# Performance work log

Hardware: AMD Instinct MI355X
Metric: run time of the kernel (lower is better)

The kernel has to match this reference:

```python
import jax, jax.numpy as jnp
import numpy as np

N_QUBITS = 3
MAX_LAYERS = 15
Q_DEPTH = 2


def _apply_ry(state, theta, axis):
    """Apply RY(theta) to qubit `axis` (axes 1..3 of state [B,2,2,2]).
    theta: scalar (shared weight) or [B] (per-sample angle). RY is real.
    """
    st = jnp.moveaxis(state, axis, 1)
    s0, s1 = st[:, 0], st[:, 1]  # [B,2,2]
    c = jnp.cos(theta / 2)
    s = jnp.sin(theta / 2)
    c = c.reshape(c.shape + (1,) * (s0.ndim - c.ndim))
    s = s.reshape(s.shape + (1,) * (s0.ndim - s.ndim))
    new = jnp.stack([c * s0 - s * s1, s * s0 + c * s1], axis=1)
    return jnp.moveaxis(new, 1, axis)


def _cnot(state, ctrl_ax, tgt_ax):
    """CNOT with control/target given as state axes (1..3): flip target where control=1."""
    st = jnp.moveaxis(state, (ctrl_ax, tgt_ax), (1, 2))
    new = jnp.stack([st[:, 0], st[:, 1, ::-1]], axis=1)
    return jnp.moveaxis(new, (1, 2), (ctrl_ax, tgt_ax))


def _quantum_circuit(q_in, q_params):
    """Batched simulation of the PennyLane q_net: H layer, RY(q_in),
    then q_depth x [entangle(CNOT(0,1),CNOT(1,2)); RY(q_weights[k+1])].
    Returns <Z_j> for j=0..2, shape [B, 3]. All gates are real-valued."""
    B = q_in.shape[0]
    qw = q_params.reshape(MAX_LAYERS, N_QUBITS)
    # Hadamards on |000> -> uniform real superposition
    state = jnp.full((B, 2, 2, 2), 1.0 / np.sqrt(8.0), dtype=q_in.dtype)
    for j in range(N_QUBITS):
        state = _apply_ry(state, q_in[:, j], j + 1)
    for k in range(Q_DEPTH):
        state = _cnot(state, 1, 2)  # CNOT(wires=[0,1])
        state = _cnot(state, 2, 3)  # CNOT(wires=[1,2])
        for j in range(N_QUBITS):
            state = _apply_ry(state, qw[k + 1, j], j + 1)
    p = state * state  # probabilities (real amplitudes)
    signs = jnp.array([1.0, -1.0], dtype=p.dtype)
    z = [jnp.sum(jnp.moveaxis(p, j + 1, 1) * signs[None, :, None, None], axis=(1, 2, 3))
         for j in range(N_QUBITS)]
    return jnp.stack(z, axis=-1)  # [B, 3]


def setup_inputs() -> dict:
    key = jax.random.key(0)
    ks = jax.random.split(key, 6)
    B, F, NQ, NOUT = 65536, 512, N_QUBITS, 100
    return {
        "input_features": jax.random.normal(ks[0], (B, F), dtype=jnp.float32),
        "pre_W": jax.random.normal(ks[1], (NQ, F), dtype=jnp.float32) * 0.04,
        "pre_b": jax.random.normal(ks[2], (NQ,), dtype=jnp.float32) * 0.04,
        "q_params": 0.01 * jax.random.normal(ks[3], (MAX_LAYERS * NQ,), dtype=jnp.float32),
        "post_W": jax.random.normal(ks[4], (NOUT, NQ), dtype=jnp.float32) * 0.5,
        "post_b": jax.random.normal(ks[5], (NOUT,), dtype=jnp.float32) * 0.5,
    }


def reference(input_features, pre_W, pre_b, q_params, post_W, post_b):
    pre_out = input_features @ pre_W.T + pre_b          # [B, 3]
    q_in = jnp.tanh(pre_out) * (np.pi / 2.0)             # [B, 3]
    q_out = _quantum_circuit(q_in, q_params)             # [B, 3]
    return q_out @ post_W.T + post_b                     # [B, 100]
```

## Files before the change

### kernel.cpp

```cpp
#include <hip/hip_runtime.h>
#include <math.h>

#define FDIM 512
#define TILE 8
#define WPB  4
#define SPB  (TILE * WPB)

#define RYPAIR(x, y, c, s) { float n0_ = (c)*(x) - (s)*(y); float n1_ = (s)*(x) + (c)*(y); (x) = n0_; (y) = n1_; }
#define SWAPF(x, y) { float t_ = (x); (x) = (y); (y) = t_; }

#define MERGE(x, y, mask) {                       \
    const bool hi_ = (lane & (mask));             \
    float keep_ = hi_ ? (y) : (x);                \
    float send_ = hi_ ? (x) : (y);                \
    (x) = keep_ + __shfl_xor(send_, (mask)); }

__global__ __launch_bounds__(256) void qnet_v3(
    const float4* __restrict__ in4,
    const float4* __restrict__ preW4,
    const float*  __restrict__ preb,
    const float*  __restrict__ qp,
    const float*  __restrict__ postW,
    const float*  __restrict__ postb,
    float2*       __restrict__ out,
    int B)
{
    const int tid  = threadIdx.x;
    const int lane = tid & 63;
    const int wave = tid >> 6;

    const float4 w0a = preW4[lane],       w0b = preW4[64 + lane];
    const float4 w1a = preW4[128 + lane], w1b = preW4[192 + lane];
    const float4 w2a = preW4[256 + lane], w2b = preW4[320 + lane];

    const float pb0 = preb[0], pb1 = preb[1], pb2 = preb[2];

    float cw[2][3], sw[2][3];
    #pragma unroll
    for (int k = 0; k < 2; ++k)
        #pragma unroll
        for (int j = 0; j < 3; ++j) {
            float th = 0.5f * qp[(k + 1) * 3 + j];
            sw[k][j] = sinf(th);
            cw[k][j] = cosf(th);
        }

    const int ol = (lane < 50) ? lane : 49;
    const float* pw = postW + 6 * ol;
    const float w00 = pw[0], w01 = pw[1], w02 = pw[2];
    const float w10 = pw[3], w11 = pw[4], w12 = pw[5];
    const float b0 = postb[2 * ol], b1 = postb[2 * ol + 1];

    const int tile_base = blockIdx.x * SPB + wave * TILE;

    float a[TILE][3];
    #pragma unroll
    for (int s = 0; s < TILE; ++s) {
        int row = tile_base + s;
        if (row >= B) row = B - 1;
        const float4* rp = in4 + (size_t)row * 128;
        float4 i0 = rp[lane];
        float4 i1 = rp[64 + lane];

        float a0 = fmaf(i0.w, w0a.w, fmaf(i0.z, w0a.z, fmaf(i0.y, w0a.y, i0.x * w0a.x)));
        a0 = fmaf(i1.w, w0b.w, fmaf(i1.z, w0b.z, fmaf(i1.y, w0b.y, fmaf(i1.x, w0b.x, a0))));
        float a1 = fmaf(i0.w, w1a.w, fmaf(i0.z, w1a.z, fmaf(i0.y, w1a.y, i0.x * w1a.x)));
        a1 = fmaf(i1.w, w1b.w, fmaf(i1.z, w1b.z, fmaf(i1.y, w1b.y, fmaf(i1.x, w1b.x, a1))));
        float a2 = fmaf(i0.w, w2a.w, fmaf(i0.z, w2a.z, fmaf(i0.y, w2a.y, i0.x * w2a.x)));
        a2 = fmaf(i1.w, w2b.w, fmaf(i1.z, w2b.z, fmaf(i1.y, w2b.y, fmaf(i1.x, w2b.x, a2))));

        a[s][0] = a0; a[s][1] = a1; a[s][2] = a2;
    }

    #pragma unroll
    for (int s = 0; s < 4; ++s) {
        #pragma unroll
        for (int j = 0; j < 3; ++j) MERGE(a[s][j], a[s + 4][j], 32);
    }
    #pragma unroll
    for (int s = 0; s < 2; ++s) {
        #pragma unroll
        for (int j = 0; j < 3; ++j) MERGE(a[s][j], a[s + 2][j], 16);
    }
    #pragma unroll
    for (int j = 0; j < 3; ++j) MERGE(a[0][j], a[1][j], 8);
    #pragma unroll
    for (int m = 4; m >= 1; m >>= 1) {
        #pragma unroll
        for (int j = 0; j < 3; ++j) a[0][j] += __shfl_xor(a[0][j], m);
    }

    float d0 = a[0][0] + pb0;
    float d1 = a[0][1] + pb1;
    float d2 = a[0][2] + pb2;

    float t0 = tanhf(d0) * 0.785398163397448f;
    float t1 = tanhf(d1) * 0.785398163397448f;
    float t2 = tanhf(d2) * 0.785398163397448f;
    float s0 = sinf(t0), c0 = cosf(t0);
    float s1 = sinf(t1), c1 = cosf(t1);
    float s2 = sinf(t2), c2 = cosf(t2);

    const float r8 = 0.353553390593274f;
    float u0m = c0 - s0, u0p = c0 + s0;
    float u1m = c1 - s1, u1p = c1 + s1;
    float u2m = (c2 - s2) * r8, u2p = (c2 + s2) * r8;
    float t00 = u0m * u1m, t01 = u0m * u1p, t10 = u0p * u1m, t11 = u0p * u1p;
    float q0 = t00 * u2m, q1 = t00 * u2p;
    float q2 = t01 * u2m, q3 = t01 * u2p;
    float q4 = t10 * u2m, q5 = t10 * u2p;
    float q6 = t11 * u2m, q7 = t11 * u2p;

    #pragma unroll
    for (int k = 0; k < 2; ++k) {
        SWAPF(q4, q6); SWAPF(q5, q7);
        SWAPF(q2, q3); SWAPF(q6, q7);
        float c = cw[k][0], s = sw[k][0];
        RYPAIR(q0, q4, c, s); RYPAIR(q1, q5, c, s); RYPAIR(q2, q6, c, s); RYPAIR(q3, q7, c, s);
        c = cw[k][1]; s = sw[k][1];
        RYPAIR(q0, q2, c, s); RYPAIR(q1, q3, c, s); RYPAIR(q4, q6, c, s); RYPAIR(q5, q7, c, s);
        c = cw[k][2]; s = sw[k][2];
        RYPAIR(q0, q1, c, s); RYPAIR(q2, q3, c, s); RYPAIR(q4, q5, c, s); RYPAIR(q6, q7, c, s);
    }

    float p0 = q0 * q0, p1 = q1 * q1, p2 = q2 * q2, p3 = q3 * q3;
    float p4 = q4 * q4, p5 = q5 * q5, p6 = q6 * q6, p7 = q7 * q7;
    float s01 = p0 + p1, s23 = p2 + p3, s45 = p4 + p5, s67 = p6 + p7;
    float z0 = (s01 + s23) - (s45 + s67);
    float z1 = (s01 - s23) + (s45 - s67);
    float z2 = (p0 - p1) + ((p2 - p3) + ((p4 - p5) + (p6 - p7)));

    #pragma unroll
    for (int s = 0; s < TILE; ++s) {
        float zz0 = __shfl(z0, 8 * s);
        float zz1 = __shfl(z1, 8 * s);
        float zz2 = __shfl(z2, 8 * s);
        int row = tile_base + s;
        float v0 = fmaf(zz2, w02, fmaf(zz1, w01, fmaf(zz0, w00, b0)));
        float v1 = fmaf(zz2, w12, fmaf(zz1, w11, fmaf(zz0, w10, b1)));
        if (lane < 50 && row < B) {
            float2 st; st.x = v0; st.y = v1;
            out[(size_t)row * 50 + lane] = st;
        }
    }
}

extern "C" void kernel_launch(void* const* d_in, const int* in_sizes, int n_in,
                              void* d_out, int out_size, void* d_ws, size_t ws_size,
                              hipStream_t stream) {
    const float4* in4   = (const float4*)d_in[0];
    const float4* preW4 = (const float4*)d_in[1];
    const float*  preb  = (const float*)d_in[2];
    const float*  qp    = (const float*)d_in[3];
    const float*  postW = (const float*)d_in[4];
    const float*  postb = (const float*)d_in[5];
    float2*       out   = (float2*)d_out;

    int B = in_sizes[0] / FDIM;
    int nblocks = (B + SPB - 1) / SPB;
    qnet_v3<<<nblocks, 256, 0, stream>>>(in4, preW4, preb, qp, postW, postb, out, B);
}
```

Measured before the change: 210.1 us.

## Use persistent grid-stride blocks with nontemporal loads and stores

Caps the grid at 1024 blocks that loop over tiles in grid-stride order, so per-block setup (weight loads, sin/cos of shared angles) is amortized over many tiles. Input rows are fetched with nontemporal loads, issued in batches of four rows before the FMAs, and outputs are written with nontemporal stores to avoid polluting cache with streaming data. Adds a launch-bounds occupancy hint. The risk is less parallelism in flight per CU, since loads are no longer spread across many short-lived blocks.

```diff
diff --git a/kernel.cpp b/kernel.cpp
--- a/kernel.cpp
+++ b/kernel.cpp
@@ -5,6 +5,10 @@
 #define TILE 8
 #define WPB  4
 #define SPB  (TILE * WPB)
+#define NBLK 1024
+
+typedef float vf4 __attribute__((ext_vector_type(4)));
+typedef float vf2 __attribute__((ext_vector_type(2)));
 
 #define RYPAIR(x, y, c, s) { float n0_ = (c)*(x) - (s)*(y); float n1_ = (s)*(x) + (c)*(y); (x) = n0_; (y) = n1_; }
 #define SWAPF(x, y) { float t_ = (x); (x) = (y); (y) = t_; }
@@ -15,7 +19,7 @@
     float send_ = hi_ ? (x) : (y);                \
     (x) = keep_ + __shfl_xor(send_, (mask)); }
 
-__global__ __launch_bounds__(256) void qnet_v3(
+__global__ __launch_bounds__(256, 4) void qnet_v4(
     const float4* __restrict__ in4,
     const float4* __restrict__ preW4,
     const float*  __restrict__ preb,
@@ -51,96 +55,110 @@
     const float w10 = pw[3], w11 = pw[4], w12 = pw[5];
     const float b0 = postb[2 * ol], b1 = postb[2 * ol + 1];
 
-    const int tile_base = blockIdx.x * SPB + wave * TILE;
+    const int tiles_per_grid = SPB * gridDim.x;
+    const int ntiles = (B + tiles_per_grid - 1) / tiles_per_grid;
 
-    float a[TILE][3];
-    #pragma unroll
-    for (int s = 0; s < TILE; ++s) {
-        int row = tile_base + s;
-        if (row >= B) row = B - 1;
-        const float4* rp = in4 + (size_t)row * 128;
-        float4 i0 = rp[lane];
-        float4 i1 = rp[64 + lane];
+    #pragma unroll 1
+    for (int t = 0; t < ntiles; ++t) {
+        const int tile_base = (blockIdx.x + t * gridDim.x) * SPB + wave * TILE;
+        if (tile_base >= B) break;
 
-        float a0 = fmaf(i0.w, w0a.w, fmaf(i0.z, w0a.z, fmaf(i0.y, w0a.y, i0.x * w0a.x)));
-        a0 = fmaf(i1.w, w0b.w, fmaf(i1.z, w0b.z, fmaf(i1.y, w0b.y, fmaf(i1.x, w0b.x, a0))));
-        float a1 = fmaf(i0.w, w1a.w, fmaf(i0.z, w1a.z, fmaf(i0.y, w1a.y, i0.x * w1a.x)));
-        a1 = fmaf(i1.w, w1b.w, fmaf(i1.z, w1b.z, fmaf(i1.y, w1b.y, fmaf(i1.x, w1b.x, a1))));
-        float a2 = fmaf(i0.w, w2a.w, fmaf(i0.z, w2a.z, fmaf(i0.y, w2a.y, i0.x * w2a.x)));
-        a2 = fmaf(i1.w, w2b.w, fmaf(i1.z, w2b.z, fmaf(i1.y, w2b.y, fmaf(i1.x, w2b.x, a2))));
+        float a[TILE][3];
+        #pragma unroll
+        for (int h = 0; h < 2; ++h) {
+            vf4 i0v[4], i1v[4];
+            #pragma unroll
+            for (int s = 0; s < 4; ++s) {
+                int row = tile_base + h * 4 + s;
+                if (row >= B) row = B - 1;
+                const vf4* rp = (const vf4*)(in4 + (size_t)row * 128);
+                i0v[s] = __builtin_nontemporal_load(rp + lane);
+                i1v[s] = __builtin_nontemporal_load(rp + 64 + lane);
+            }
+            #pragma unroll
+            for (int s = 0; s < 4; ++s) {
+                const vf4 i0 = i0v[s], i1 = i1v[s];
+                float a0 = fmaf(i0.w, w0a.w, fmaf(i0.z, w0a.z, fmaf(i0.y, w0a.y, i0.x * w0a.x)));
+                a0 = fmaf(i1.w, w0b.w, fmaf(i1.z, w0b.z, fmaf(i1.y, w0b.y, fmaf(i1.x, w0b.x, a0))));
+                float a1 = fmaf(i0.w, w1a.w, fmaf(i0.z, w1a.z, fmaf(i0.y, w1a.y, i0.x * w1a.x)));
+                a1 = fmaf(i1.w, w1b.w, fmaf(i1.z, w1b.z, fmaf(i1.y, w1b.y, fmaf(i1.x, w1b.x, a1))));
+                float a2 = fmaf(i0.w, w2a.w, fmaf(i0.z, w2a.z, fmaf(i0.y, w2a.y, i0.x * w2a.x)));
+                a2 = fmaf(i1.w, w2b.w, fmaf(i1.z, w2b.z, fmaf(i1.y, w2b.y, fmaf(i1.x, w2b.x, a2))));
+                a[h * 4 + s][0] = a0; a[h * 4 + s][1] = a1; a[h * 4 + s][2] = a2;
+            }
+        }
 
-        a[s][0] = a0; a[s][1] = a1; a[s][2] = a2;
-    }
+        #pragma unroll
+        for (int s = 0; s < 4; ++s) {
+            #pragma unroll
+            for (int j = 0; j < 3; ++j) MERGE(a[s][j], a[s + 4][j], 32);
+        }
+        #pragma unroll
+        for (int s = 0; s < 2; ++s) {
+            #pragma unroll
+            for (int j = 0; j < 3; ++j) MERGE(a[s][j], a[s + 2][j], 16);
+        }
+        #pragma unroll
+        for (int j = 0; j < 3; ++j) MERGE(a[0][j], a[1][j], 8);
+        #pragma unroll
+        for (int m = 4; m >= 1; m >>= 1) {
+            #pragma unroll
+            for (int j = 0; j < 3; ++j) a[0][j] += __shfl_xor(a[0][j], m);
+        }
 
-    #pragma unroll
-    for (int s = 0; s < 4; ++s) {
+        float d0 = a[0][0] + pb0;
+        float d1 = a[0][1] + pb1;
+        float d2 = a[0][2] + pb2;
+
+        float t0 = tanhf(d0) * 0.785398163397448f;
+        float t1 = tanhf(d1) * 0.785398163397448f;
+        float t2 = tanhf(d2) * 0.785398163397448f;
+        float s0 = sinf(t0), c0 = cosf(t0);
+        float s1 = sinf(t1), c1 = cosf(t1);
+        float s2 = sinf(t2), c2 = cosf(t2);
+
+        const float r8 = 0.353553390593274f;
+        float u0m = c0 - s0, u0p = c0 + s0;
+        float u1m = c1 - s1, u1p = c1 + s1;
+        float u2m = (c2 - s2) * r8, u2p = (c2 + s2) * r8;
+        float t00 = u0m * u1m, t01 = u0m * u1p, t10 = u0p * u1m, t11 = u0p * u1p;
+        float q0 = t00 * u2m, q1 = t00 * u2p;
+        float q2 = t01 * u2m, q3 = t01 * u2p;
+        float q4 = t10 * u2m, q5 = t10 * u2p;
+        float q6 = t11 * u2m, q7 = t11 * u2p;
+
         #pragma unroll
-        for (int j = 0; j < 3; ++j) MERGE(a[s][j], a[s + 4][j], 32);
-    }
-    #pragma unroll
-    for (int s = 0; s < 2; ++s) {
+        for (int k = 0; k < 2; ++k) {
+            SWAPF(q4, q6); SWAPF(q5, q7);
+            SWAPF(q2, q3); SWAPF(q6, q7);
+            float c = cw[k][0], s = sw[k][0];
+            RYPAIR(q0, q4, c, s); RYPAIR(q1, q5, c, s); RYPAIR(q2, q6, c, s); RYPAIR(q3, q7, c, s);
+            c = cw[k][1]; s = sw[k][1];
+            RYPAIR(q0, q2, c, s); RYPAIR(q1, q3, c, s); RYPAIR(q4, q6, c, s); RYPAIR(q5, q7, c, s);
+            c = cw[k][2]; s = sw[k][2];
+            RYPAIR(q0, q1, c, s); RYPAIR(q2, q3, c, s); RYPAIR(q4, q5, c, s); RYPAIR(q6, q7, c, s);
+        }
+
+        float p0 = q0 * q0, p1 = q1 * q1, p2 = q2 * q2, p3 = q3 * q3;
+        float p4 = q4 * q4, p5 = q5 * q5, p6 = q6 * q6, p7 = q7 * q7;
+        float s01 = p0 + p1, s23 = p2 + p3, s45 = p4 + p5, s67 = p6 + p7;
+        float z0 = (s01 + s23) - (s45 + s67);
+        float z1 = (s01 - s23) + (s45 - s67);
+        float z2 = (p0 - p1) + ((p2 - p3) + ((p4 - p5) + (p6 - p7)));
+
         #pragma unroll
-        for (int j = 0; j < 3; ++j) MERGE(a[s][j], a[s + 2][j], 16);
-    }
-    #pragma unroll
-    for (int j = 0; j < 3; ++j) MERGE(a[0][j], a[1][j], 8);
-    #pragma unroll
-    for (int m = 4; m >= 1; m >>= 1) {
-        #pragma unroll
-        for (int j = 0; j < 3; ++j) a[0][j] += __shfl_xor(a[0][j], m);
-    }
-
-    float d0 = a[0][0] + pb0;
-    float d1 = a[0][1] + pb1;
-    float d2 = a[0][2] + pb2;
-
-    float t0 = tanhf(d0) * 0.785398163397448f;
-    float t1 = tanhf(d1) * 0.785398163397448f;
-    float t2 = tanhf(d2) * 0.785398163397448f;
-    float s0 = sinf(t0), c0 = cosf(t0);
-    float s1 = sinf(t1), c1 = cosf(t1);
-    float s2 = sinf(t2), c2 = cosf(t2);
-
-    const float r8 = 0.353553390593274f;
-    float u0m = c0 - s0, u0p = c0 + s0;
-    float u1m = c1 - s1, u1p = c1 + s1;
-    float u2m = (c2 - s2) * r8, u2p = (c2 + s2) * r8;
-    float t00 = u0m * u1m, t01 = u0m * u1p, t10 = u0p * u1m, t11 = u0p * u1p;
-    float q0 = t00 * u2m, q1 = t00 * u2p;
-    float q2 = t01 * u2m, q3 = t01 * u2p;
-    float q4 = t10 * u2m, q5 = t10 * u2p;
-    float q6 = t11 * u2m, q7 = t11 * u2p;
-
-    #pragma unroll
-    for (int k = 0; k < 2; ++k) {
-        SWAPF(q4, q6); SWAPF(q5, q7);
-        SWAPF(q2, q3); SWAPF(q6, q7);
-        float c = cw[k][0], s = sw[k][0];
-        RYPAIR(q0, q4, c, s); RYPAIR(q1, q5, c, s); RYPAIR(q2, q6, c, s); RYPAIR(q3, q7, c, s);
-        c = cw[k][1]; s = sw[k][1];
-        RYPAIR(q0, q2, c, s); RYPAIR(q1, q3, c, s); RYPAIR(q4, q6, c, s); RYPAIR(q5, q7, c, s);
-        c = cw[k][2]; s = sw[k][2];
-        RYPAIR(q0, q1, c, s); RYPAIR(q2, q3, c, s); RYPAIR(q4, q5, c, s); RYPAIR(q6, q7, c, s);
-    }
-
-    float p0 = q0 * q0, p1 = q1 * q1, p2 = q2 * q2, p3 = q3 * q3;
-    float p4 = q4 * q4, p5 = q5 * q5, p6 = q6 * q6, p7 = q7 * q7;
-    float s01 = p0 + p1, s23 = p2 + p3, s45 = p4 + p5, s67 = p6 + p7;
-    float z0 = (s01 + s23) - (s45 + s67);
-    float z1 = (s01 - s23) + (s45 - s67);
-    float z2 = (p0 - p1) + ((p2 - p3) + ((p4 - p5) + (p6 - p7)));
-
-    #pragma unroll
-    for (int s = 0; s < TILE; ++s) {
-        float zz0 = __shfl(z0, 8 * s);
-        float zz1 = __shfl(z1, 8 * s);
-        float zz2 = __shfl(z2, 8 * s);
-        int row = tile_base + s;
-        float v0 = fmaf(zz2, w02, fmaf(zz1, w01, fmaf(zz0, w00, b0)));
-        float v1 = fmaf(zz2, w12, fmaf(zz1, w11, fmaf(zz0, w10, b1)));
-        if (lane < 50 && row < B) {
-            float2 st; st.x = v0; st.y = v1;
-            out[(size_t)row * 50 + lane] = st;
+        for (int s = 0; s < TILE; ++s) {
+            float zz0 = __shfl(z0, 8 * s);
+            float zz1 = __shfl(z1, 8 * s);
+            float zz2 = __shfl(z2, 8 * s);
+            int row = tile_base + s;
+            float v0 = fmaf(zz2, w02, fmaf(zz1, w01, fmaf(zz0, w00, b0)));
+            float v1 = fmaf(zz2, w12, fmaf(zz1, w11, fmaf(zz0, w10, b1)));
+            if (lane < 50 && row < B) {
+                vf2 st; st.x = v0; st.y = v1;
+                vf2* op = (vf2*)(out + (size_t)row * 50 + lane);
+                __builtin_nontemporal_store(st, op);
+            }
         }
     }
 }
@@ -157,6 +175,7 @@
     float2*       out   = (float2*)d_out;
 
     int B = in_sizes[0] / FDIM;
-    int nblocks = (B + SPB - 1) / SPB;
-    qnet_v3<<<nblocks, 256, 0, stream>>>(in4, preW4, preb, qp, postW, postb, out, B);
+    int maxblocks = (B + SPB - 1) / SPB;
+    int nblocks = maxblocks < NBLK ? maxblocks : NBLK;
+    qnet_v4<<<nblocks, 256, 0, stream>>>(in4, preW4, preb, qp, postW, postb, out, B);
 }
```

Measured after the change: 199.9 us. 4.9% less time.

## Make kernel persistent with grid-stride loop and software-pipelined nontemporal loads

Applied to the files above, without the earlier changes.

Replaces one-tile-per-wave blocks with a persistent grid of up to 768 blocks that loop over tiles with a grid stride. The next tile's input rows are prefetched into registers while the current tile's dot products run, and loads and stores use nontemporal hints. sinf/cosf become the fast __sinf/__cosf intrinsics. The aim is to keep more memory requests in flight and cut block launch overhead, at the cost of more register pressure. Rows at the tail are no longer clamped, so correctness relies on B being a multiple of 8 (tb+4 is loaded without a bounds check).

```diff
diff --git a/kernel.cpp b/kernel.cpp
--- a/kernel.cpp
+++ b/kernel.cpp
@@ -5,6 +5,10 @@
 #define TILE 8
 #define WPB  4
 #define SPB  (TILE * WPB)
+#define NBLK 768
+
+typedef float vf4 __attribute__((ext_vector_type(4)));
+typedef float vf2 __attribute__((ext_vector_type(2)));
 
 #define RYPAIR(x, y, c, s) { float n0_ = (c)*(x) - (s)*(y); float n1_ = (s)*(x) + (c)*(y); (x) = n0_; (y) = n1_; }
 #define SWAPF(x, y) { float t_ = (x); (x) = (y); (y) = t_; }
@@ -15,7 +19,28 @@
     float send_ = hi_ ? (x) : (y);                \
     (x) = keep_ + __shfl_xor(send_, (mask)); }
 
-__global__ __launch_bounds__(256) void qnet_v3(
+#define LOADH(baserow, D0, D1) {                                              \
+    _Pragma("unroll")                                                         \
+    for (int s_ = 0; s_ < 4; ++s_) {                                          \
+        const vf4* rp_ = (const vf4*)(in4 + (size_t)((baserow) + s_) * 128);  \
+        D0[s_] = __builtin_nontemporal_load(rp_ + lane);                      \
+        D1[s_] = __builtin_nontemporal_load(rp_ + 64 + lane);                 \
+    } }
+
+#define FMA4(D0, D1, off) {                                                                 \
+    _Pragma("unroll")                                                                       \
+    for (int s_ = 0; s_ < 4; ++s_) {                                                        \
+        const vf4 i0 = D0[s_], i1 = D1[s_];                                                 \
+        float a0 = fmaf(i0.w, w0a.w, fmaf(i0.z, w0a.z, fmaf(i0.y, w0a.y, i0.x * w0a.x)));   \
+        a0 = fmaf(i1.w, w0b.w, fmaf(i1.z, w0b.z, fmaf(i1.y, w0b.y, fmaf(i1.x, w0b.x, a0))));\
+        float a1 = fmaf(i0.w, w1a.w, fmaf(i0.z, w1a.z, fmaf(i0.y, w1a.y, i0.x * w1a.x)));   \
+        a1 = fmaf(i1.w, w1b.w, fmaf(i1.z, w1b.z, fmaf(i1.y, w1b.y, fmaf(i1.x, w1b.x, a1))));\
+        float a2 = fmaf(i0.w, w2a.w, fmaf(i0.z, w2a.z, fmaf(i0.y, w2a.y, i0.x * w2a.x)));   \
+        a2 = fmaf(i1.w, w2b.w, fmaf(i1.z, w2b.z, fmaf(i1.y, w2b.y, fmaf(i1.x, w2b.x, a2))));\
+        a[(off) + s_][0] = a0; a[(off) + s_][1] = a1; a[(off) + s_][2] = a2;                \
+    } }
+
+__global__ __launch_bounds__(256) void qnet_v5(
     const float4* __restrict__ in4,
     const float4* __restrict__ preW4,
     const float*  __restrict__ preb,
@@ -51,97 +76,98 @@
     const float w10 = pw[3], w11 = pw[4], w12 = pw[5];
     const float b0 = postb[2 * ol], b1 = postb[2 * ol + 1];
 
-    const int tile_base = blockIdx.x * SPB + wave * TILE;
+    const int stride = SPB * gridDim.x;
+    int tb = blockIdx.x * SPB + wave * TILE;
+    if (tb >= B) return;
 
-    float a[TILE][3];
-    #pragma unroll
-    for (int s = 0; s < TILE; ++s) {
-        int row = tile_base + s;
-        if (row >= B) row = B - 1;
-        const float4* rp = in4 + (size_t)row * 128;
-        float4 i0 = rp[lane];
-        float4 i1 = rp[64 + lane];
+    vf4 X0[4], X1[4];
+    vf4 Y0[4], Y1[4];
+    LOADH(tb, X0, X1);
 
-        float a0 = fmaf(i0.w, w0a.w, fmaf(i0.z, w0a.z, fmaf(i0.y, w0a.y, i0.x * w0a.x)));
-        a0 = fmaf(i1.w, w0b.w, fmaf(i1.z, w0b.z, fmaf(i1.y, w0b.y, fmaf(i1.x, w0b.x, a0))));
-        float a1 = fmaf(i0.w, w1a.w, fmaf(i0.z, w1a.z, fmaf(i0.y, w1a.y, i0.x * w1a.x)));
-        a1 = fmaf(i1.w, w1b.w, fmaf(i1.z, w1b.z, fmaf(i1.y, w1b.y, fmaf(i1.x, w1b.x, a1))));
-        float a2 = fmaf(i0.w, w2a.w, fmaf(i0.z, w2a.z, fmaf(i0.y, w2a.y, i0.x * w2a.x)));
-        a2 = fmaf(i1.w, w2b.w, fmaf(i1.z, w2b.z, fmaf(i1.y, w2b.y, fmaf(i1.x, w2b.x, a2))));
+    #pragma unroll 1
+    for (;;) {
+        float a[TILE][3];
+        LOADH(tb + 4, Y0, Y1);
+        FMA4(X0, X1, 0);
+        const int tbn = tb + stride;
+        if (tbn < B) LOADH(tbn, X0, X1);
+        FMA4(Y0, Y1, 4);
 
-        a[s][0] = a0; a[s][1] = a1; a[s][2] = a2;
-    }
+        #pragma unroll
+        for (int s = 0; s < 4; ++s) {
+            #pragma unroll
+            for (int j = 0; j < 3; ++j) MERGE(a[s][j], a[s + 4][j], 32);
+        }
+        #pragma unroll
+        for (int s = 0; s < 2; ++s) {
+            #pragma unroll
+            for (int j = 0; j < 3; ++j) MERGE(a[s][j], a[s + 2][j], 16);
+        }
+        #pragma unroll
+        for (int j = 0; j < 3; ++j) MERGE(a[0][j], a[1][j], 8);
+        #pragma unroll
+        for (int m = 4; m >= 1; m >>= 1) {
+            #pragma unroll
+            for (int j = 0; j < 3; ++j) a[0][j] += __shfl_xor(a[0][j], m);
+        }
 
-    #pragma unroll
-    for (int s = 0; s < 4; ++s) {
+        float d0 = a[0][0] + pb0;
+        float d1 = a[0][1] + pb1;
+        float d2 = a[0][2] + pb2;
+
+        float t0 = tanhf(d0) * 0.785398163397448f;
+        float t1 = tanhf(d1) * 0.785398163397448f;
+        float t2 = tanhf(d2) * 0.785398163397448f;
+        float s0 = __sinf(t0), c0 = __cosf(t0);
+        float s1 = __sinf(t1), c1 = __cosf(t1);
+        float s2 = __sinf(t2), c2 = __cosf(t2);
+
+        const float r8 = 0.353553390593274f;
+        float u0m = c0 - s0, u0p = c0 + s0;
+        float u1m = c1 - s1, u1p = c1 + s1;
+        float u2m = (c2 - s2) * r8, u2p = (c2 + s2) * r8;
+        float t00 = u0m * u1m, t01 = u0m * u1p, t10 = u0p * u1m, t11 = u0p * u1p;
+        float q0 = t00 * u2m, q1 = t00 * u2p;
+        float q2 = t01 * u2m, q3 = t01 * u2p;
+        float q4 = t10 * u2m, q5 = t10 * u2p;
+        float q6 = t11 * u2m, q7 = t11 * u2p;
+
         #pragma unroll
-        for (int j = 0; j < 3; ++j) MERGE(a[s][j], a[s + 4][j], 32);
-    }
-    #pragma unroll
-    for (int s = 0; s < 2; ++s) {
+        for (int k = 0; k < 2; ++k) {
+            SWAPF(q4, q6); SWAPF(q5, q7);
+            SWAPF(q2, q3); SWAPF(q6, q7);
+            float c = cw[k][0], s = sw[k][0];
+            RYPAIR(q0, q4, c, s); RYPAIR(q1, q5, c, s); RYPAIR(q2, q6, c, s); RYPAIR(q3, q7, c, s);
+            c = cw[k][1]; s = sw[k][1];
+            RYPAIR(q0, q2, c, s); RYPAIR(q1, q3, c, s); RYPAIR(q4, q6, c, s); RYPAIR(q5, q7, c, s);
+            c = cw[k][2]; s = sw[k][2];
+            RYPAIR(q0, q1, c, s); RYPAIR(q2, q3, c, s); RYPAIR(q4, q5, c, s); RYPAIR(q6, q7, c, s);
+        }
+
+        float p0 = q0 * q0, p1 = q1 * q1, p2 = q2 * q2, p3 = q3 * q3;
+        float p4 = q4 * q4, p5 = q5 * q5, p6 = q6 * q6, p7 = q7 * q7;
+        float s01 = p0 + p1, s23 = p2 + p3, s45 = p4 + p5, s67 = p6 + p7;
+        float z0 = (s01 + s23) - (s45 + s67);
+        float z1 = (s01 - s23) + (s45 - s67);
+        float z2 = (p0 - p1) + ((p2 - p3) + ((p4 - p5) + (p6 - p7)));
+
         #pragma unroll
-        for (int j = 0; j < 3; ++j) MERGE(a[s][j], a[s + 2][j], 16);
-    }
-    #pragma unroll
-    for (int j = 0; j < 3; ++j) MERGE(a[0][j], a[1][j], 8);
-    #pragma unroll
-    for (int m = 4; m >= 1; m >>= 1) {
-        #pragma unroll
-        for (int j = 0; j < 3; ++j) a[0][j] += __shfl_xor(a[0][j], m);
-    }
+        for (int s = 0; s < TILE; ++s) {
+            float zz0 = __shfl(z0, 8 * s);
+            float zz1 = __shfl(z1, 8 * s);
+            float zz2 = __shfl(z2, 8 * s);
+            int row = tb + s;
+            float v0 = fmaf(zz2, w02, fmaf(zz1, w01, fmaf(zz0, w00, b0)));
+            float v1 = fmaf(zz2, w12, fmaf(zz1, w11, fmaf(zz0, w10, b1)));
+            if (lane < 50 && row < B) {
+                vf2 st; st.x = v0; st.y = v1;
+                vf2* op = (vf2*)(out + (size_t)row * 50 + lane);
+                __builtin_nontemporal_store(st, op);
+            }
+        }
 
-    float d0 = a[0][0] + pb0;
-    float d1 = a[0][1] + pb1;
-    float d2 = a[0][2] + pb2;
-
-    float t0 = tanhf(d0) * 0.785398163397448f;
-    float t1 = tanhf(d1) * 0.785398163397448f;
-    float t2 = tanhf(d2) * 0.785398163397448f;
-    float s0 = sinf(t0), c0 = cosf(t0);
-    float s1 = sinf(t1), c1 = cosf(t1);
-    float s2 = sinf(t2), c2 = cosf(t2);
-
-    const float r8 = 0.353553390593274f;
-    float u0m = c0 - s0, u0p = c0 + s0;
-    float u1m = c1 - s1, u1p = c1 + s1;
-    float u2m = (c2 - s2) * r8, u2p = (c2 + s2) * r8;
-    float t00 = u0m * u1m, t01 = u0m * u1p, t10 = u0p * u1m, t11 = u0p * u1p;
-    float q0 = t00 * u2m, q1 = t00 * u2p;
-    float q2 = t01 * u2m, q3 = t01 * u2p;
-    float q4 = t10 * u2m, q5 = t10 * u2p;
-    float q6 = t11 * u2m, q7 = t11 * u2p;
-
-    #pragma unroll
-    for (int k = 0; k < 2; ++k) {
-        SWAPF(q4, q6); SWAPF(q5, q7);
-        SWAPF(q2, q3); SWAPF(q6, q7);
-        float c = cw[k][0], s = sw[k][0];
-        RYPAIR(q0, q4, c, s); RYPAIR(q1, q5, c, s); RYPAIR(q2, q6, c, s); RYPAIR(q3, q7, c, s);
-        c = cw[k][1]; s = sw[k][1];
-        RYPAIR(q0, q2, c, s); RYPAIR(q1, q3, c, s); RYPAIR(q4, q6, c, s); RYPAIR(q5, q7, c, s);
-        c = cw[k][2]; s = sw[k][2];
-        RYPAIR(q0, q1, c, s); RYPAIR(q2, q3, c, s); RYPAIR(q4, q5, c, s); RYPAIR(q6, q7, c, s);
-    }
-
-    float p0 = q0 * q0, p1 = q1 * q1, p2 = q2 * q2, p3 = q3 * q3;
-    float p4 = q4 * q4, p5 = q5 * q5, p6 = q6 * q6, p7 = q7 * q7;
-    float s01 = p0 + p1, s23 = p2 + p3, s45 = p4 + p5, s67 = p6 + p7;
-    float z0 = (s01 + s23) - (s45 + s67);
-    float z1 = (s01 - s23) + (s45 - s67);
-    float z2 = (p0 - p1) + ((p2 - p3) + ((p4 - p5) + (p6 - p7)));
-
-    #pragma unroll
-    for (int s = 0; s < TILE; ++s) {
-        float zz0 = __shfl(z0, 8 * s);
-        float zz1 = __shfl(z1, 8 * s);
-        float zz2 = __shfl(z2, 8 * s);
-        int row = tile_base + s;
-        float v0 = fmaf(zz2, w02, fmaf(zz1, w01, fmaf(zz0, w00, b0)));
-        float v1 = fmaf(zz2, w12, fmaf(zz1, w11, fmaf(zz0, w10, b1)));
-        if (lane < 50 && row < B) {
-            float2 st; st.x = v0; st.y = v1;
-            out[(size_t)row * 50 + lane] = st;
-        }
+        if (tbn >= B) break;
+        tb = tbn;
     }
 }
 
@@ -157,6 +183,7 @@
     float2*       out   = (float2*)d_out;
 
     int B = in_sizes[0] / FDIM;
-    int nblocks = (B + SPB - 1) / SPB;
-    qnet_v3<<<nblocks, 256, 0, stream>>>(in4, preW4, preb, qp, postW, postb, out, B);
+    int maxblocks = (B + SPB - 1) / SPB;
+    int nblocks = maxblocks < NBLK ? maxblocks : NBLK;
+    qnet_v5<<<nblocks, 256, 0, stream>>>(in4, preW4, preb, qp, postW, postb, out, B);
 }
```

Result: faster. 197.5 us (-6.0%).
